# Performance work log

Hardware: AMD Instinct MI355X
Metric: run time of the kernel (lower is better)

The kernel has to match this reference:

```python
import jax, jax.numpy as jnp
import numpy as np

N_EMBED = 64
HEAD_SIZE = 64
B, T = 4096, 128

def setup_inputs() -> dict:
    key = jax.random.key(0)
    k0, k1, k2, k3 = jax.random.split(key, 4)
    x = jax.random.normal(k0, (B, T, N_EMBED), dtype=jnp.float32)
    # nn.Linear(N_EMBED, head_size, bias=False): weight shape [head_size, N_EMBED], y = x @ W.T
    Wq = jax.random.normal(k1, (HEAD_SIZE, N_EMBED), dtype=jnp.float32) * (1.0 / np.sqrt(N_EMBED))
    Wk = jax.random.normal(k2, (HEAD_SIZE, N_EMBED), dtype=jnp.float32) * (1.0 / np.sqrt(N_EMBED))
    Wv = jax.random.normal(k3, (HEAD_SIZE, N_EMBED), dtype=jnp.float32) * (1.0 / np.sqrt(N_EMBED))
    return {"x": x, "Wq": Wq, "Wk": Wk, "Wv": Wv}

def reference(x, Wq, Wk, Wv):
    # q,k,v: [B,T,H]
    q = jnp.einsum('btc,hc->bth', x, Wq)
    k = jnp.einsum('btc,hc->bth', x, Wk)
    v = jnp.einsum('btc,hc->bth', x, Wv)
    scale = HEAD_SIZE ** -0.5
    scores = jnp.einsum('bth,bsh->bts', q, k) * scale  # [B,T,T]
    Tdim = x.shape[1]
    causal = jnp.tril(jnp.ones((Tdim, Tdim), dtype=bool))
    scores = jnp.where(causal, scores, -jnp.inf)
    weights = jax.nn.softmax(scores, axis=-1)
    # dropout disabled (eval mode) for deterministic reference
    out = jnp.einsum('bts,bsh->bth', weights, v)  # [B,T,H]
    return out
```

## Files before the change

kernel.cpp:

```cpp
#include <hip/hip_runtime.h>

#define KS 76
#define VS 140

typedef float f4  __attribute__((ext_vector_type(4)));
typedef short s8v __attribute__((ext_vector_type(8)));
typedef short s4v __attribute__((ext_vector_type(4)));

#define MFMA16(a, b, c) __builtin_amdgcn_mfma_f32_16x16x32_bf16((a), (b), (c), 0, 0, 0)

__device__ __forceinline__ unsigned short f2bf(float f) {
  union { float f; unsigned u; } x; x.f = f;
  unsigned r = x.u + 0x7FFFu + ((x.u >> 16) & 1u);
  return (unsigned short)(r >> 16);
}
__device__ __forceinline__ float bf2f(unsigned short s) {
  union { unsigned u; float f; } x; x.u = ((unsigned)s) << 16; return x.f;
}
__device__ __forceinline__ s8v cvt8(const float* p) {
  float4 a = *(const float4*)p;
  float4 b = *(const float4*)(p + 4);
  s8v v;
  v[0] = (short)f2bf(a.x); v[1] = (short)f2bf(a.y);
  v[2] = (short)f2bf(a.z); v[3] = (short)f2bf(a.w);
  v[4] = (short)f2bf(b.x); v[5] = (short)f2bf(b.y);
  v[6] = (short)f2bf(b.z); v[7] = (short)f2bf(b.w);
  return v;
}
__device__ __forceinline__ s8v ld8(const short* p) {
  s4v lo = *(const s4v*)p;
  s4v hi = *(const s4v*)(p + 4);
  s8v r;
  r[0] = lo[0]; r[1] = lo[1]; r[2] = lo[2]; r[3] = lo[3];
  r[4] = hi[0]; r[5] = hi[1]; r[6] = hi[2]; r[7] = hi[3];
  return r;
}
__device__ __forceinline__ unsigned pack2(float a, float b) {
  return (unsigned)f2bf(a) | ((unsigned)f2bf(b) << 16);
}

__device__ __forceinline__ s8v qshuf(unsigned pa0, unsigned pa1,
                                     unsigned pb0, unsigned pb1,
                                     int s0, bool hi) {
  int a0 = __shfl((int)pa0, s0);
  int a1 = __shfl((int)pa1, s0);
  int a2 = __shfl((int)pa0, s0 + 16);
  int a3 = __shfl((int)pa1, s0 + 16);
  int b0 = __shfl((int)pb0, s0);
  int b1 = __shfl((int)pb1, s0);
  int b2 = __shfl((int)pb0, s0 + 16);
  int b3 = __shfl((int)pb1, s0 + 16);
  union { int u[4]; s8v v; } r;
  r.u[0] = hi ? b0 : a0;
  r.u[1] = hi ? b1 : a1;
  r.u[2] = hi ? b2 : a2;
  r.u[3] = hi ? b3 : a3;
  return r.v;
}

__global__ void detect_bf16(const unsigned short* __restrict__ w, int nelems,
                            int* __restrict__ flag) {
  __shared__ int cnt;
  if (threadIdx.x == 0) cnt = 0;
  __syncthreads();
  int local = 0;
  for (int i = threadIdx.x; i < nelems; i += blockDim.x) {
    float f = bf2f(w[i]);
    float a = fabsf(f);
    if (f == 0.0f || (a >= 1e-4f && a <= 1e4f)) local++;
  }
  atomicAdd(&cnt, local);
  __syncthreads();
  if (threadIdx.x == 0) *flag = (cnt >= (nelems / 10) * 9) ? 1 : 0;
}

__global__ __launch_bounds__(256, 3)
void attn_head(const void* __restrict__ xg, const void* __restrict__ wqg,
               const void* __restrict__ wkg, const void* __restrict__ wvg,
               void* __restrict__ outg, const int* __restrict__ flagp) {
  __shared__ __align__(16) short smem[18688];
  short* Ksm = smem;
  short* Vt  = smem + 9728;

  const int tid  = threadIdx.x;
  const int wave = tid >> 6;
  const int lane = tid & 63;
  const int c16  = lane & 15;
  const int quad = lane >> 4;
  const int b    = blockIdx.x;
  const int isbf = *flagp;
  const int mts[2] = {wave, 7 - wave};

  s8v xf[2][2];
  #pragma unroll
  for (int mi = 0; mi < 2; mi++) {
    const size_t base = (size_t)b * (128 * 64) + (size_t)(mts[mi] * 16 + c16) * 64;
    #pragma unroll
    for (int kt = 0; kt < 2; kt++) {
      const int off = kt * 32 + quad * 8;
      if (isbf) xf[mi][kt] = *(const s8v*)((const unsigned short*)xg + base + off);
      else      xf[mi][kt] = cvt8((const float*)xg + base + off);
    }
  }

  f4 QT[2][4];
  #pragma unroll
  for (int ht = 0; ht < 4; ht++) {
    s8v wqf[2], wkf[2], wvf[2];
    const int woff0 = (ht * 16 + c16) * 64 + quad * 8;
    #pragma unroll
    for (int kt = 0; kt < 2; kt++) {
      const int off = woff0 + kt * 32;
      if (isbf) {
        wqf[kt] = *(const s8v*)((const unsigned short*)wqg + off);
        wkf[kt] = *(const s8v*)((const unsigned short*)wkg + off);
        wvf[kt] = *(const s8v*)((const unsigned short*)wvg + off);
      } else {
        wqf[kt] = cvt8((const float*)wqg + off);
        wkf[kt] = cvt8((const float*)wkg + off);
        wvf[kt] = cvt8((const float*)wvg + off);
      }
    }
    #pragma unroll
    for (int mi = 0; mi < 2; mi++) {
      const int m = mts[mi];
      f4 z = {0.f, 0.f, 0.f, 0.f};
      f4 qt = z, kk = z, vv = z;
      qt = MFMA16(wqf[0], xf[mi][0], qt);  qt = MFMA16(wqf[1], xf[mi][1], qt);
      kk = MFMA16(xf[mi][0], wkf[0], kk);  kk = MFMA16(xf[mi][1], wkf[1], kk);
      vv = MFMA16(xf[mi][0], wvf[0], vv);  vv = MFMA16(xf[mi][1], wvf[1], vv);
      QT[mi][ht] = qt;
      #pragma unroll
      for (int r = 0; r < 4; r++)
        Ksm[(m * 16 + quad * 4 + r) * KS + ht * 16 + c16] = (short)f2bf(kk[r]);
      s4v pv;
      pv[0] = (short)f2bf(vv[0]); pv[1] = (short)f2bf(vv[1]);
      pv[2] = (short)f2bf(vv[2]); pv[3] = (short)f2bf(vv[3]);
      *(s4v*)(Vt + (ht * 16 + c16) * VS + m * 16 + quad * 4) = pv;
    }
  }
  __syncthreads();

  const int s0 = ((quad & 1) * 2) * 16 + c16;
  const bool hi = quad >= 2;

  #pragma unroll
  for (int mi = 0; mi < 2; mi++) {
    const int m = mts[mi];
    unsigned qpk[4][2];
    #pragma unroll
    for (int ht = 0; ht < 4; ht++) {
      qpk[ht][0] = pack2(QT[mi][ht][0] * 0.125f, QT[mi][ht][1] * 0.125f);
      qpk[ht][1] = pack2(QT[mi][ht][2] * 0.125f, QT[mi][ht][3] * 0.125f);
    }
    s8v qb[2];
    qb[0] = qshuf(qpk[0][0], qpk[0][1], qpk[1][0], qpk[1][1], s0, hi);
    qb[1] = qshuf(qpk[2][0], qpk[2][1], qpk[3][0], qpk[3][1], s0, hi);

    f4 S[8];
    #pragma unroll
    for (int nt = 0; nt < 8; nt++) {
      if (nt > m) continue;
      const s8v ka0 = ld8(Ksm + (nt * 16 + c16) * KS + quad * 8);
      const s8v ka1 = ld8(Ksm + (nt * 16 + c16) * KS + 32 + quad * 8);
      f4 s = {0.f, 0.f, 0.f, 0.f};
      s = MFMA16(ka0, qb[0], s);
      s = MFMA16(ka1, qb[1], s);
      S[nt] = s;
    }
    float sum = 0.f;
    #pragma unroll
    for (int nt = 0; nt < 8; nt++) {
      if (nt > m) continue;
      #pragma unroll
      for (int r = 0; r < 4; r++) {
        const bool keep = (nt < m) || (quad * 4 + r <= c16);
        float e = keep ? __expf(S[nt][r]) : 0.0f;
        S[nt][r] = e;
        sum += e;
      }
    }
    sum += __shfl_xor(sum, 16);
    sum += __shfl_xor(sum, 32);
    const float inv = 1.0f / sum;

    unsigned ppk[8][2];
    #pragma unroll
    for (int nt = 0; nt < 8; nt++) {
      if (nt > m) continue;
      ppk[nt][0] = pack2(S[nt][0], S[nt][1]);
      ppk[nt][1] = pack2(S[nt][2], S[nt][3]);
    }

    f4 acc[4];
    #pragma unroll
    for (int ht = 0; ht < 4; ht++) { f4 z = {0.f,0.f,0.f,0.f}; acc[ht] = z; }
    const int nchunk = (m >> 1) + 1;
    #pragma unroll
    for (int kt = 0; kt < 4; kt++) {
      if (kt >= nchunk) continue;
      const bool hb = (2 * kt + 1) <= m;
      s8v pb = qshuf(ppk[2 * kt][0], ppk[2 * kt][1],
                     hb ? ppk[2 * kt + 1][0] : 0u,
                     hb ? ppk[2 * kt + 1][1] : 0u, s0, hi);
      #pragma unroll
      for (int ht = 0; ht < 4; ht++) {
        const s8v va = ld8(Vt + (ht * 16 + c16) * VS + kt * 32 + quad * 8);
        acc[ht] = MFMA16(va, pb, acc[ht]);
      }
    }

    if (isbf) {
      unsigned short* op = (unsigned short*)outg + (size_t)b * (128 * 64);
      #pragma unroll
      for (int ht = 0; ht < 4; ht++) {
        s4v o;
        o[0] = (short)f2bf(acc[ht][0] * inv); o[1] = (short)f2bf(acc[ht][1] * inv);
        o[2] = (short)f2bf(acc[ht][2] * inv); o[3] = (short)f2bf(acc[ht][3] * inv);
        *(s4v*)(op + (size_t)(m * 16 + c16) * 64 + ht * 16 + quad * 4) = o;
      }
    } else {
      float* op = (float*)outg + (size_t)b * (128 * 64);
      #pragma unroll
      for (int ht = 0; ht < 4; ht++) {
        float4 o = {acc[ht][0] * inv, acc[ht][1] * inv,
                    acc[ht][2] * inv, acc[ht][3] * inv};
        *(float4*)(op + (size_t)(m * 16 + c16) * 64 + ht * 16 + quad * 4) = o;
      }
    }
  }
}

extern "C" void kernel_launch(void* const* d_in, const int* in_sizes, int n_in,
                              void* d_out, int out_size, void* d_ws, size_t ws_size,
                              hipStream_t stream) {
  int* flag = (int*)d_ws;
  detect_bf16<<<dim3(1), dim3(256), 0, stream>>>(
      (const unsigned short*)d_in[1], in_sizes[1], flag);
  attn_head<<<dim3(4096), dim3(256), 0, stream>>>(
      d_in[0], d_in[1], d_in[2], d_in[3], d_out, (const int*)flag);
}
```

Before: 313.0 us.

## Permute K-dim operand layout to drop shuffles and inline dtype detection

Removes the cross-lane shuffles that rearranged packed Q and P fragments into MFMA B-operand layout. Instead it relies on a permuted reduction-index order, loading K and V rows as two 4-element pieces strided by 16 so they match the accumulator's native layout. It also drops the separate bf16-detection kernel launch and computes the dtype flag in each block with __syncthreads_count over 256 weight samples. The extra per-block check adds a global read and a barrier in exchange for one fewer launch and no dependency on a workspace flag.

Result: no change. 316.2 us (+1.0%).

```diff
diff --git a/kernel.cpp b/kernel.cpp
--- a/kernel.cpp
+++ b/kernel.cpp
@@ -27,57 +27,27 @@
   v[6] = (short)f2bf(b.z); v[7] = (short)f2bf(b.w);
   return v;
 }
-__device__ __forceinline__ s8v ld8(const short* p) {
-  s4v lo = *(const s4v*)p;
-  s4v hi = *(const s4v*)(p + 4);
-  s8v r;
-  r[0] = lo[0]; r[1] = lo[1]; r[2] = lo[2]; r[3] = lo[3];
-  r[4] = hi[0]; r[5] = hi[1]; r[6] = hi[2]; r[7] = hi[3];
-  return r;
-}
 __device__ __forceinline__ unsigned pack2(float a, float b) {
   return (unsigned)f2bf(a) | ((unsigned)f2bf(b) << 16);
 }
-
-__device__ __forceinline__ s8v qshuf(unsigned pa0, unsigned pa1,
-                                     unsigned pb0, unsigned pb1,
-                                     int s0, bool hi) {
-  int a0 = __shfl((int)pa0, s0);
-  int a1 = __shfl((int)pa1, s0);
-  int a2 = __shfl((int)pa0, s0 + 16);
-  int a3 = __shfl((int)pa1, s0 + 16);
-  int b0 = __shfl((int)pb0, s0);
-  int b1 = __shfl((int)pb1, s0);
-  int b2 = __shfl((int)pb0, s0 + 16);
-  int b3 = __shfl((int)pb1, s0 + 16);
-  union { int u[4]; s8v v; } r;
-  r.u[0] = hi ? b0 : a0;
-  r.u[1] = hi ? b1 : a1;
-  r.u[2] = hi ? b2 : a2;
-  r.u[3] = hi ? b3 : a3;
+__device__ __forceinline__ s8v mk8(unsigned a0, unsigned a1, unsigned b0, unsigned b1) {
+  union { unsigned u[4]; s8v v; } r;
+  r.u[0] = a0; r.u[1] = a1; r.u[2] = b0; r.u[3] = b1;
   return r.v;
 }
-
-__global__ void detect_bf16(const unsigned short* __restrict__ w, int nelems,
-                            int* __restrict__ flag) {
-  __shared__ int cnt;
-  if (threadIdx.x == 0) cnt = 0;
-  __syncthreads();
-  int local = 0;
-  for (int i = threadIdx.x; i < nelems; i += blockDim.x) {
-    float f = bf2f(w[i]);
-    float a = fabsf(f);
-    if (f == 0.0f || (a >= 1e-4f && a <= 1e4f)) local++;
-  }
-  atomicAdd(&cnt, local);
-  __syncthreads();
-  if (threadIdx.x == 0) *flag = (cnt >= (nelems / 10) * 9) ? 1 : 0;
+__device__ __forceinline__ s8v ld44(const short* p0, const short* p1) {
+  s4v a = *(const s4v*)p0;
+  s4v b = *(const s4v*)(p1);
+  s8v r;
+  r[0] = a[0]; r[1] = a[1]; r[2] = a[2]; r[3] = a[3];
+  r[4] = b[0]; r[5] = b[1]; r[6] = b[2]; r[7] = b[3];
+  return r;
 }
 
 __global__ __launch_bounds__(256, 3)
 void attn_head(const void* __restrict__ xg, const void* __restrict__ wqg,
                const void* __restrict__ wkg, const void* __restrict__ wvg,
-               void* __restrict__ outg, const int* __restrict__ flagp) {
+               void* __restrict__ outg) {
   __shared__ __align__(16) short smem[18688];
   short* Ksm = smem;
   short* Vt  = smem + 9728;
@@ -88,7 +58,16 @@
   const int c16  = lane & 15;
   const int quad = lane >> 4;
   const int b    = blockIdx.x;
-  const int isbf = *flagp;
+
+  int ok;
+  {
+    const unsigned short* w = (const unsigned short*)wqg;
+    float f = bf2f(w[tid]);
+    float a = fabsf(f);
+    ok = (f == 0.0f || (a >= 1e-4f && a <= 1e4f)) ? 1 : 0;
+  }
+  const int isbf = (__syncthreads_count(ok) >= 230) ? 1 : 0;
+
   const int mts[2] = {wave, 7 - wave};
 
   s8v xf[2][2];
@@ -139,35 +118,35 @@
       *(s4v*)(Vt + (ht * 16 + c16) * VS + m * 16 + quad * 4) = pv;
     }
   }
+
+  s8v qb[2][2];
+  #pragma unroll
+  for (int mi = 0; mi < 2; mi++)
+    #pragma unroll
+    for (int hp = 0; hp < 2; hp++)
+      qb[mi][hp] = mk8(
+          pack2(QT[mi][2*hp][0]   * 0.125f, QT[mi][2*hp][1]   * 0.125f),
+          pack2(QT[mi][2*hp][2]   * 0.125f, QT[mi][2*hp][3]   * 0.125f),
+          pack2(QT[mi][2*hp+1][0] * 0.125f, QT[mi][2*hp+1][1] * 0.125f),
+          pack2(QT[mi][2*hp+1][2] * 0.125f, QT[mi][2*hp+1][3] * 0.125f));
+
   __syncthreads();
-
-  const int s0 = ((quad & 1) * 2) * 16 + c16;
-  const bool hi = quad >= 2;
 
   #pragma unroll
   for (int mi = 0; mi < 2; mi++) {
     const int m = mts[mi];
-    unsigned qpk[4][2];
-    #pragma unroll
-    for (int ht = 0; ht < 4; ht++) {
-      qpk[ht][0] = pack2(QT[mi][ht][0] * 0.125f, QT[mi][ht][1] * 0.125f);
-      qpk[ht][1] = pack2(QT[mi][ht][2] * 0.125f, QT[mi][ht][3] * 0.125f);
-    }
-    s8v qb[2];
-    qb[0] = qshuf(qpk[0][0], qpk[0][1], qpk[1][0], qpk[1][1], s0, hi);
-    qb[1] = qshuf(qpk[2][0], qpk[2][1], qpk[3][0], qpk[3][1], s0, hi);
 
     f4 S[8];
     #pragma unroll
     for (int nt = 0; nt < 8; nt++) {
       if (nt > m) continue;
-      const s8v ka0 = ld8(Ksm + (nt * 16 + c16) * KS + quad * 8);
-      const s8v ka1 = ld8(Ksm + (nt * 16 + c16) * KS + 32 + quad * 8);
+      const short* kr = Ksm + (nt * 16 + c16) * KS + quad * 4;
       f4 s = {0.f, 0.f, 0.f, 0.f};
-      s = MFMA16(ka0, qb[0], s);
-      s = MFMA16(ka1, qb[1], s);
+      s = MFMA16(ld44(kr,      kr + 16), qb[mi][0], s);
+      s = MFMA16(ld44(kr + 32, kr + 48), qb[mi][1], s);
       S[nt] = s;
     }
+
     float sum = 0.f;
     #pragma unroll
     for (int nt = 0; nt < 8; nt++) {
@@ -200,13 +179,13 @@
     for (int kt = 0; kt < 4; kt++) {
       if (kt >= nchunk) continue;
       const bool hb = (2 * kt + 1) <= m;
-      s8v pb = qshuf(ppk[2 * kt][0], ppk[2 * kt][1],
-                     hb ? ppk[2 * kt + 1][0] : 0u,
-                     hb ? ppk[2 * kt + 1][1] : 0u, s0, hi);
+      const s8v pb = mk8(ppk[2 * kt][0], ppk[2 * kt][1],
+                         hb ? ppk[2 * kt + 1][0] : 0u,
+                         hb ? ppk[2 * kt + 1][1] : 0u);
       #pragma unroll
       for (int ht = 0; ht < 4; ht++) {
-        const s8v va = ld8(Vt + (ht * 16 + c16) * VS + kt * 32 + quad * 8);
-        acc[ht] = MFMA16(va, pb, acc[ht]);
+        const short* vr = Vt + (ht * 16 + c16) * VS + kt * 32 + quad * 4;
+        acc[ht] = MFMA16(ld44(vr, vr + 16), pb, acc[ht]);
       }
     }
 
@@ -234,9 +213,7 @@
 extern "C" void kernel_launch(void* const* d_in, const int* in_sizes, int n_in,
                               void* d_out, int out_size, void* d_ws, size_t ws_size,
                               hipStream_t stream) {
-  int* flag = (int*)d_ws;
-  detect_bf16<<<dim3(1), dim3(256), 0, stream>>>(
-      (const unsigned short*)d_in[1], in_sizes[1], flag);
+  (void)d_ws; (void)ws_size; (void)in_sizes; (void)n_in; (void)out_size;
   attn_head<<<dim3(4096), dim3(256), 0, stream>>>(
-      d_in[0], d_in[1], d_in[2], d_in[3], d_out, (const int*)flag);
-}
+      d_in[0], d_in[1], d_in[2], d_in[3], d_out);
+}
```
